# Optimization experiments

Hardware: AMD Instinct MI355X
Metric: run time of the kernel (lower is better)

The kernel has to match this reference:

```python
import jax, jax.numpy as jnp
import numpy as np

B, S, HID = 4, 1024, 1024
NH, NKV, HD = 16, 8, 64
EPS = 1e-6
ROPE_BASE = 10000.0


def setup_inputs() -> dict:
    key = jax.random.key(0)
    ks = jax.random.split(key, 6)
    hidden_states = jax.random.normal(ks[0], (B, S, HID), jnp.float32)
    # RoPE tables: cos/sin of shape [B, S, HD] (half-frequency layout, duplicated)
    inv_freq = 1.0 / (ROPE_BASE ** (jnp.arange(0, HD, 2, dtype=jnp.float32) / HD))
    pos = jnp.arange(S, dtype=jnp.float32)
    freqs = pos[:, None] * inv_freq[None, :]              # [S, HD/2]
    emb = jnp.concatenate([freqs, freqs], axis=-1)         # [S, HD]
    cos = jnp.broadcast_to(jnp.cos(emb)[None], (B, S, HD))
    sin = jnp.broadcast_to(jnp.sin(emb)[None], (B, S, HD))
    # additive causal mask [B, 1, S, S]
    causal = jnp.where(jnp.tril(jnp.ones((S, S), bool)), 0.0, -1e9).astype(jnp.float32)
    attention_mask = jnp.broadcast_to(causal[None, None], (B, 1, S, S))
    sc = 0.02
    Wq = jax.random.normal(ks[1], (NH * HD, HID), jnp.float32) * sc
    Wk = jax.random.normal(ks[2], (NKV * HD, HID), jnp.float32) * sc
    Wv = jax.random.normal(ks[3], (NKV * HD, HID), jnp.float32) * sc
    Wo = jax.random.normal(ks[4], (HID, NH * HD), jnp.float32) * sc
    q_norm_w = jnp.ones((HD,), jnp.float32)
    k_norm_w = jnp.ones((HD,), jnp.float32)
    return {"hidden_states": hidden_states, "cos": cos, "sin": sin,
            "attention_mask": attention_mask, "Wq": Wq, "Wk": Wk, "Wv": Wv,
            "Wo": Wo, "q_norm_w": q_norm_w, "k_norm_w": k_norm_w}


def _rms_norm(x, w):
    dt = x.dtype
    x32 = x.astype(jnp.float32)
    var = jnp.mean(x32 * x32, axis=-1, keepdims=True)
    x32 = x32 * jax.lax.rsqrt(var + EPS)
    return w * x32.astype(dt)


def _rotate_half(x):
    x1, x2 = jnp.split(x, 2, axis=-1)
    return jnp.concatenate([-x2, x1], axis=-1)


def reference(hidden_states, cos, sin, attention_mask, Wq, Wk, Wv, Wo, q_norm_w, k_norm_w):
    b, s, _ = hidden_states.shape
    scaling = HD ** -0.5
    # QKV projections (bias=False), reshape to heads, per-head RMSNorm on q/k
    q = (hidden_states @ Wq.T).reshape(b, s, NH, HD)
    k = (hidden_states @ Wk.T).reshape(b, s, NKV, HD)
    v = (hidden_states @ Wv.T).reshape(b, s, NKV, HD)
    q = _rms_norm(q, q_norm_w).transpose(0, 2, 1, 3)   # [B, NH, S, HD]
    k = _rms_norm(k, k_norm_w).transpose(0, 2, 1, 3)   # [B, NKV, S, HD]
    v = v.transpose(0, 2, 1, 3)                         # [B, NKV, S, HD]
    # RoPE (unsqueeze_dim=1 -> broadcast over heads)
    c = cos[:, None, :, :]
    sn = sin[:, None, :, :]
    q = q * c + _rotate_half(q) * sn
    k = k * c + _rotate_half(k) * sn
    # GQA: repeat kv heads
    groups = NH // NKV
    k = jnp.repeat(k, groups, axis=1)
    v = jnp.repeat(v, groups, axis=1)
    # eager attention
    scores = jnp.einsum('bhqd,bhkd->bhqk', q, k) * scaling + attention_mask
    attn_weights = jax.nn.softmax(scores.astype(jnp.float32), axis=-1).astype(q.dtype)
    ctx = jnp.einsum('bhqk,bhkd->bhqd', attn_weights, v)
    ctx = ctx.transpose(0, 2, 1, 3).reshape(b, s, NH * HD)
    out = ctx @ Wo.T
    return (out, attn_weights)
```

## Files before the change

kernel.cpp:

```cpp
#include <hip/hip_runtime.h>
#include <hip/hip_fp16.h>

#define Bb 4
#define Ss 1024
#define HID 1024
#define NH 16
#define NKV 8
#define HD 64

typedef _Float16 f16x8 __attribute__((ext_vector_type(8)));
typedef _Float16 f16x4 __attribute__((ext_vector_type(4)));
typedef float f32x4 __attribute__((ext_vector_type(4)));

typedef const __attribute__((address_space(1))) unsigned int gu32;
typedef __attribute__((address_space(3))) unsigned int lu32;

__device__ __forceinline__ void gl_lds16(const _Float16* g, _Float16* l) {
  __builtin_amdgcn_global_load_lds((gu32*)g, (lu32*)l, 16, 0, 0);
}

__global__ __launch_bounds__(256) void f2h_all(
    const float* __restrict__ a0, const float* __restrict__ a1,
    const float* __restrict__ a2, const float* __restrict__ a3,
    const float* __restrict__ a4, _Float16* __restrict__ o0,
    _Float16* __restrict__ o1, _Float16* __restrict__ o2,
    _Float16* __restrict__ o3, _Float16* __restrict__ o4) {
  const int bid = blockIdx.x;
  const float* src;
  _Float16* dst;
  int base;
  if (bid < 4096)      { src = a0; dst = o0; base = bid; }
  else if (bid < 5120) { src = a1; dst = o1; base = bid - 4096; }
  else if (bid < 5632) { src = a2; dst = o2; base = bid - 5120; }
  else if (bid < 6144) { src = a3; dst = o3; base = bid - 5632; }
  else                 { src = a4; dst = o4; base = bid - 6144; }
  const int i = base * 1024 + threadIdx.x * 4;
  const float4 v = *(const float4*)(src + i);
  f16x4 h;
  h[0] = (_Float16)v.x; h[1] = (_Float16)v.y;
  h[2] = (_Float16)v.z; h[3] = (_Float16)v.w;
  *(f16x4*)(dst + i) = h;
}

template <int EPI>
__global__ __launch_bounds__(256) void gemm128(
    const _Float16* __restrict__ A, const _Float16* __restrict__ Bt,
    float* __restrict__ C, _Float16* __restrict__ qh, _Float16* __restrict__ kh,
    _Float16* __restrict__ vTp, const float* __restrict__ qnw,
    const float* __restrict__ knw, const float* __restrict__ cosd,
    const float* __restrict__ sind, int N, int K) {
  __shared__ __align__(16) _Float16 As[128][64];
  __shared__ __align__(16) _Float16 Bs[128][64];
  const int tid = threadIdx.x;
  const int wave = tid >> 6, lane = tid & 63;
  const int lr = lane & 15, lk = lane >> 4;
  const int wr = wave >> 1, wc = wave & 1;
  const int bm = blockIdx.x * 128;
  const int by = blockIdx.y;
  const int bn = by * 128;

  f32x4 acc[4][4] = {};

  const _Float16* asrc[4];
  const _Float16* bsrc[4];
  _Float16 *adst[4], *bdst[4];
#pragma unroll
  for (int i = 0; i < 4; ++i) {
    const int ch = i * 256 + tid;
    const int r = ch >> 3, ccl = ch & 7;
    const int ccg = ccl ^ (r & 7);
    asrc[i] = A + (size_t)(bm + r) * K + ccg * 8;
    bsrc[i] = Bt + (size_t)(bn + r) * K + ccg * 8;
    adst[i] = &As[0][0] + ch * 8;
    bdst[i] = &Bs[0][0] + ch * 8;
  }

  for (int k0 = 0; k0 < K; k0 += 64) {
    __syncthreads();
#pragma unroll
    for (int i = 0; i < 4; ++i) {
      gl_lds16(asrc[i] + k0, adst[i]);
      gl_lds16(bsrc[i] + k0, bdst[i]);
    }
    __syncthreads();
#pragma unroll
    for (int kk = 0; kk < 2; ++kk) {
      f16x8 af[4], bf[4];
#pragma unroll
      for (int m = 0; m < 4; ++m) {
        const int r = wr * 64 + m * 16 + lr;
        const int s = (kk * 4 + lk) ^ (r & 7);
        af[m] = *(const f16x8*)(&As[r][0] + s * 8);
      }
#pragma unroll
      for (int n = 0; n < 4; ++n) {
        const int r = wc * 64 + n * 16 + lr;
        const int s = (kk * 4 + lk) ^ (r & 7);
        bf[n] = *(const f16x8*)(&Bs[r][0] + s * 8);
      }
#pragma unroll
      for (int m = 0; m < 4; ++m)
#pragma unroll
        for (int n = 0; n < 4; ++n)
          acc[m][n] =
              __builtin_amdgcn_mfma_f32_16x16x32_f16(af[m], bf[n], acc[m][n], 0, 0, 0);
    }
  }

  if (EPI == 0) {
#pragma unroll
    for (int m = 0; m < 4; ++m) {
      const int row = bm + wr * 64 + m * 16 + lk * 4;
#pragma unroll
      for (int n = 0; n < 4; ++n) {
        const int c = bn + wc * 64 + n * 16 + lr;
#pragma unroll
        for (int j = 0; j < 4; ++j)
          C[(size_t)(row + j) * N + c] = acc[m][n][j];
      }
    }
  } else {
    const int b = bm >> 10;
    const int s0 = bm & 1023;
    const int hd2 = by * 2 + wc;
    if (hd2 < 24) {
      const bool isQ = (hd2 < 16);
      const float* nw = isQ ? qnw : knw;
      _Float16* dst = isQ ? qh : kh;
      const int ncols = isQ ? (NH * HD) : (NKV * HD);
      const int hcol = (isQ ? hd2 : (hd2 - 16)) * HD;
      float nwv[4];
#pragma unroll
      for (int n = 0; n < 4; ++n) nwv[n] = nw[n * 16 + lr];
#pragma unroll
      for (int m = 0; m < 4; ++m) {
#pragma unroll
        for (int j = 0; j < 4; ++j) {
          const int row = bm + wr * 64 + m * 16 + lk * 4 + j;
          float ss = 0.f;
#pragma unroll
          for (int n = 0; n < 4; ++n) ss += acc[m][n][j] * acc[m][n][j];
#pragma unroll
          for (int o = 1; o < 16; o <<= 1) ss += __shfl_xor(ss, o);
          const float rs = rsqrtf(ss * (1.0f / 64.0f) + 1e-6f);
          float y[4];
#pragma unroll
          for (int n = 0; n < 4; ++n) y[n] = acc[m][n][j] * rs * nwv[n];
          const size_t rb = (size_t)row * HD;
#pragma unroll
          for (int n = 0; n < 4; ++n) {
            const int d = n * 16 + lr;
            const float rot = (n < 2) ? -y[n + 2] : y[n - 2];
            dst[(size_t)row * ncols + hcol + d] =
                (_Float16)(y[n] * cosd[rb + d] + rot * sind[rb + d]);
          }
        }
      }
    } else {
      const int kv = hd2 - 24;
#pragma unroll
      for (int m = 0; m < 4; ++m) {
        const int sbase = s0 + wr * 64 + m * 16 + lk * 4;
#pragma unroll
        for (int n = 0; n < 4; ++n) {
          const int d = n * 16 + lr;
          f16x4 pk;
#pragma unroll
          for (int j = 0; j < 4; ++j) pk[j] = (_Float16)acc[m][n][j];
          *(f16x4*)&vTp[((size_t)((b * NKV + kv) * HD + d)) * Ss + sbase] = pk;
        }
      }
    }
  }
}

__global__ __launch_bounds__(256) void gemm_oproj(
    const _Float16* __restrict__ A, const _Float16* __restrict__ Bt,
    float* __restrict__ C, int N, int K) {
  __shared__ __align__(16) _Float16 As[128][64];
  __shared__ __align__(16) _Float16 Bs[64][64];
  const int tid = threadIdx.x;
  const int wave = tid >> 6, lane = tid & 63;
  const int lr = lane & 15, lk = lane >> 4;
  const int bm = blockIdx.x * 128;
  const int bn = blockIdx.y * 64;

  f32x4 acc[2][4] = {};

  const _Float16* asrc[4];
  const _Float16* bsrc[2];
  _Float16 *adst[4], *bdst[2];
#pragma unroll
  for (int i = 0; i < 4; ++i) {
    const int ch = i * 256 + tid;
    const int r = ch >> 3, ccl = ch & 7;
    const int ccg = ccl ^ (r & 7);
    asrc[i] = A + (size_t)(bm + r) * K + ccg * 8;
    adst[i] = &As[0][0] + ch * 8;
  }
#pragma unroll
  for (int i = 0; i < 2; ++i) {
    const int ch = i * 256 + tid;
    const int r = ch >> 3, ccl = ch & 7;
    const int ccg = ccl ^ (r & 7);
    bsrc[i] = Bt + (size_t)(bn + r) * K + ccg * 8;
    bdst[i] = &Bs[0][0] + ch * 8;
  }

  for (int k0 = 0; k0 < K; k0 += 64) {
    __syncthreads();
#pragma unroll
    for (int i = 0; i < 4; ++i) gl_lds16(asrc[i] + k0, adst[i]);
#pragma unroll
    for (int i = 0; i < 2; ++i) gl_lds16(bsrc[i] + k0, bdst[i]);
    __syncthreads();
#pragma unroll
    for (int kk = 0; kk < 2; ++kk) {
      f16x8 af[2], bf[4];
#pragma unroll
      for (int m = 0; m < 2; ++m) {
        const int r = wave * 32 + m * 16 + lr;
        const int s = (kk * 4 + lk) ^ (r & 7);
        af[m] = *(const f16x8*)(&As[r][0] + s * 8);
      }
#pragma unroll
      for (int n = 0; n < 4; ++n) {
        const int r = n * 16 + lr;
        const int s = (kk * 4 + lk) ^ (r & 7);
        bf[n] = *(const f16x8*)(&Bs[r][0] + s * 8);
      }
#pragma unroll
      for (int m = 0; m < 2; ++m)
#pragma unroll
        for (int n = 0; n < 4; ++n)
          acc[m][n] =
              __builtin_amdgcn_mfma_f32_16x16x32_f16(af[m], bf[n], acc[m][n], 0, 0, 0);
    }
  }
#pragma unroll
  for (int m = 0; m < 2; ++m) {
    const int row = bm + wave * 32 + m * 16 + lk * 4;
#pragma unroll
    for (int n = 0; n < 4; ++n) {
      const int c = bn + n * 16 + lr;
#pragma unroll
      for (int j = 0; j < 4; ++j)
        C[(size_t)(row + j) * N + c] = acc[m][n][j];
    }
  }
}

__global__ __launch_bounds__(256) void attn_kernel(
    const _Float16* __restrict__ qh, const _Float16* __restrict__ kh,
    const _Float16* __restrict__ vT, float* __restrict__ attn,
    _Float16* __restrict__ ctxh) {
  __shared__ __align__(16) _Float16 Ks[64][72];
  __shared__ __align__(16) _Float16 Vs[64][72];
  __shared__ __align__(16) _Float16 Wh[4][16][72];
  const int x = blockIdx.x, h = blockIdx.y, b = blockIdx.z;
  int qt;
  switch (b) {
    case 0:  qt = x; break;
    case 1:  qt = 15 - x; break;
    case 2:  qt = (x + 8) & 15; break;
    default: qt = (7 - x) & 15; break;
  }
  const int kvh = h >> 1;
  const int tid = threadIdx.x, wave = tid >> 6, lane = tid & 63;
  const int lr = lane & 15, lk = lane >> 4;
  const int q0 = qt * 64, qrow0 = q0 + wave * 16;
  float* attn_bh = attn + (size_t)(b * NH + h) * Ss * Ss;

  const int sr = tid >> 3, sc = tid & 7;
  const _Float16* kb0 = kh + (size_t)(b * Ss) * (NKV * HD) + kvh * HD + sc * 8;
  const _Float16* vb0 = vT + (size_t)((b * NKV + kvh) * HD) * Ss + sc * 8;

  const _Float16* qp = qh + (size_t)(b * Ss + qrow0 + lr) * (NH * HD) + h * HD + lk * 8;
  const f16x8 aq0 = *(const f16x8*)qp;
  const f16x8 aq1 = *(const f16x8*)(qp + 32);

  const float C1 = 0.18033688011112042f;
  const float C2 = -11.541560327111707f;

  f16x8 pk0 = *(const f16x8*)(kb0 + (size_t)sr * (NKV * HD));
  f16x8 pk1 = *(const f16x8*)(kb0 + (size_t)(sr + 32) * (NKV * HD));
  float lsum[4] = {0.f, 0.f, 0.f, 0.f};
  for (int t = 0; t <= qt; ++t) {
    __syncthreads();
    *(f16x8*)&Ks[sr][sc * 8] = pk0;
    *(f16x8*)&Ks[sr + 32][sc * 8] = pk1;
    if (t < qt) {
      pk0 = *(const f16x8*)(kb0 + (size_t)((t + 1) * 64 + sr) * (NKV * HD));
      pk1 = *(const f16x8*)(kb0 + (size_t)((t + 1) * 64 + sr + 32) * (NKV * HD));
    }
    __syncthreads();
    f32x4 acc[4] = {};
#pragma unroll
    for (int n = 0; n < 4; ++n) {
      f16x8 b0 = *(const f16x8*)&Ks[n * 16 + lr][lk * 8];
      acc[n] = __builtin_amdgcn_mfma_f32_16x16x32_f16(aq0, b0, acc[n], 0, 0, 0);
    }
#pragma unroll
    for (int n = 0; n < 4; ++n) {
      f16x8 b1 = *(const f16x8*)&Ks[n * 16 + lr][32 + lk * 8];
      acc[n] = __builtin_amdgcn_mfma_f32_16x16x32_f16(aq1, b1, acc[n], 0, 0, 0);
    }
    if (t < qt) {
#pragma unroll
      for (int j = 0; j < 4; ++j)
#pragma unroll
        for (int n = 0; n < 4; ++n) lsum[j] += exp2f(fmaf(acc[n][j], C1, C2));
    } else {
#pragma unroll
      for (int j = 0; j < 4; ++j) {
        const int gr = qrow0 + lk * 4 + j;
#pragma unroll
        for (int n = 0; n < 4; ++n) {
          float p = exp2f(fmaf(acc[n][j], C1, C2));
          if (q0 + n * 16 + lr > gr) p = 0.f;
          lsum[j] += p;
        }
      }
    }
  }
  float linv[4];
#pragma unroll
  for (int j = 0; j < 4; ++j) {
#pragma unroll
    for (int o = 1; o < 16; o <<= 1) lsum[j] += __shfl_xor(lsum[j], o);
    linv[j] = 1.0f / lsum[j];
  }

  pk0 = *(const f16x8*)(kb0 + (size_t)sr * (NKV * HD));
  pk1 = *(const f16x8*)(kb0 + (size_t)(sr + 32) * (NKV * HD));
  f16x8 pv0 = *(const f16x8*)(vb0 + (size_t)sr * Ss);
  f16x8 pv1 = *(const f16x8*)(vb0 + (size_t)(sr + 32) * Ss);
  f32x4 acc2[4] = {};
  const int wr2 = lane >> 4;
  const int wc2 = (lane & 15) * 4;
  for (int t = 0; t <= qt; ++t) {
    __syncthreads();
    *(f16x8*)&Ks[sr][sc * 8] = pk0;
    *(f16x8*)&Ks[sr + 32][sc * 8] = pk1;
    *(f16x8*)&Vs[sr][sc * 8] = pv0;
    *(f16x8*)&Vs[sr + 32][sc * 8] = pv1;
    if (t < qt) {
      pk0 = *(const f16x8*)(kb0 + (size_t)((t + 1) * 64 + sr) * (NKV * HD));
      pk1 = *(const f16x8*)(kb0 + (size_t)((t + 1) * 64 + sr + 32) * (NKV * HD));
      pv0 = *(const f16x8*)(vb0 + (size_t)sr * Ss + (t + 1) * 64);
      pv1 = *(const f16x8*)(vb0 + (size_t)(sr + 32) * Ss + (t + 1) * 64);
    }
    __syncthreads();
    f32x4 acc[4] = {};
#pragma unroll
    for (int n = 0; n < 4; ++n) {
      f16x8 b0 = *(const f16x8*)&Ks[n * 16 + lr][lk * 8];
      acc[n] = __builtin_amdgcn_mfma_f32_16x16x32_f16(aq0, b0, acc[n], 0, 0, 0);
    }
#pragma unroll
    for (int n = 0; n < 4; ++n) {
      f16x8 b1 = *(const f16x8*)&Ks[n * 16 + lr][32 + lk * 8];
      acc[n] = __builtin_amdgcn_mfma_f32_16x16x32_f16(aq1, b1, acc[n], 0, 0, 0);
    }
    if (t < qt) {
#pragma unroll
      for (int j = 0; j < 4; ++j)
#pragma unroll
        for (int n = 0; n < 4; ++n) {
          const float w = exp2f(fmaf(acc[n][j], C1, C2)) * linv[j];
          Wh[wave][lk * 4 + j][n * 16 + lr] = (_Float16)w;
        }
    } else {
#pragma unroll
      for (int j = 0; j < 4; ++j) {
        const int gr = qrow0 + lk * 4 + j;
#pragma unroll
        for (int n = 0; n < 4; ++n) {
          float w = exp2f(fmaf(acc[n][j], C1, C2)) * linv[j];
          if (q0 + n * 16 + lr > gr) w = 0.f;
          Wh[wave][lk * 4 + j][n * 16 + lr] = (_Float16)w;
        }
      }
    }
#pragma unroll
    for (int kc = 0; kc < 2; ++kc) {
      f16x8 aw = *(const f16x8*)&Wh[wave][lr][kc * 32 + lk * 8];
#pragma unroll
      for (int n = 0; n < 4; ++n) {
        f16x8 bv = *(const f16x8*)&Vs[n * 16 + lr][kc * 32 + lk * 8];
        acc2[n] = __builtin_amdgcn_mfma_f32_16x16x32_f16(aw, bv, acc2[n], 0, 0, 0);
      }
    }
#pragma unroll
    for (int i2 = 0; i2 < 4; ++i2) {
      f16x4 hv = *(const f16x4*)&Wh[wave][wr2 + i2 * 4][wc2];
      *(float4*)&attn_bh[(size_t)(qrow0 + wr2 + i2 * 4) * Ss + t * 64 + wc2] =
          make_float4((float)hv[0], (float)hv[1], (float)hv[2], (float)hv[3]);
    }
  }

  for (int t = qt + 1; t < 16; ++t)
    for (int idx = tid; idx < 1024; idx += 256) {
      int r = idx >> 4, c4 = (idx & 15) * 4;
      *(float4*)&attn_bh[(size_t)(q0 + r) * Ss + t * 64 + c4] =
          make_float4(0.f, 0.f, 0.f, 0.f);
    }

#pragma unroll
  for (int n = 0; n < 4; ++n)
#pragma unroll
    for (int j = 0; j < 4; ++j)
      ctxh[(size_t)(b * Ss + qrow0 + lk * 4 + j) * (NH * HD) + h * HD + n * 16 + lr] =
          (_Float16)acc2[n][j];
}

extern "C" void kernel_launch(void* const* d_in, const int* in_sizes, int n_in,
                              void* d_out, int out_size, void* d_ws, size_t ws_size,
                              hipStream_t stream) {
  const float* hs   = (const float*)d_in[0];
  const float* cosb = (const float*)d_in[1];
  const float* sinb = (const float*)d_in[2];
  const float* Wq = (const float*)d_in[4];
  const float* Wk = (const float*)d_in[5];
  const float* Wv = (const float*)d_in[6];
  const float* Wo = (const float*)d_in[7];
  const float* qw = (const float*)d_in[8];
  const float* kw = (const float*)d_in[9];

  char* ws = (char*)d_ws;
  _Float16* Xh    = (_Float16*)(ws);
  _Float16* Wqkvh = (_Float16*)(ws + 8388608);
  _Float16* Woh   = (_Float16*)(ws + 12582912);
  _Float16* qh    = (_Float16*)(ws + 14680064);
  _Float16* kh    = (_Float16*)(ws + 23068672);
  _Float16* vT    = (_Float16*)(ws + 27262976);
  _Float16* ctxh  = (_Float16*)(ws + 31457280);

  float* out  = (float*)d_out;
  float* attn = out + (size_t)Bb * Ss * HID;

  f2h_all<<<7168, 256, 0, stream>>>(hs, Wq, Wk, Wv, Wo, Xh, Wqkvh,
                                    Wqkvh + 1048576, Wqkvh + 1572864, Woh);

  gemm128<1><<<dim3(32, 16), 256, 0, stream>>>(
      Xh, Wqkvh, nullptr, qh, kh, vT, qw, kw, cosb, sinb, 2048, 1024);

  attn_kernel<<<dim3(16, 16, 4), 256, 0, stream>>>(qh, kh, vT, attn, ctxh);

  gemm_oproj<<<dim3(32, 16), 256, 0, stream>>>(ctxh, Woh, out, 1024, 1024);
}
```

Before: 132.4 us.

## Share K/V tiles across GQA head pair in one 512-thread attention block

```diff
diff --git a/kernel.cpp b/kernel.cpp
--- a/kernel.cpp
+++ b/kernel.cpp
@@ -250,30 +250,30 @@
   }
 }
 
-__global__ __launch_bounds__(256) void attn_kernel(
+__global__ __launch_bounds__(512) void attn_kernel(
     const _Float16* __restrict__ qh, const _Float16* __restrict__ kh,
     const _Float16* __restrict__ vT, float* __restrict__ attn,
     _Float16* __restrict__ ctxh) {
   __shared__ __align__(16) _Float16 Ks[64][72];
   __shared__ __align__(16) _Float16 Vs[64][72];
-  __shared__ __align__(16) _Float16 Wh[4][16][72];
-  const int x = blockIdx.x, h = blockIdx.y, b = blockIdx.z;
+  __shared__ __align__(16) _Float16 Wh[8][16][72];
+  const int x = blockIdx.x, g = blockIdx.y, b = blockIdx.z;
   int qt;
   switch (b) {
     case 0:  qt = x; break;
-    case 1:  qt = 15 - x; break;
-    case 2:  qt = (x + 8) & 15; break;
+    case 1:  qt = (x + 8) & 15; break;
+    case 2:  qt = 15 - x; break;
     default: qt = (7 - x) & 15; break;
   }
-  const int kvh = h >> 1;
   const int tid = threadIdx.x, wave = tid >> 6, lane = tid & 63;
   const int lr = lane & 15, lk = lane >> 4;
-  const int q0 = qt * 64, qrow0 = q0 + wave * 16;
+  const int h = 2 * g + (wave >> 2);
+  const int q0 = qt * 64, qrow0 = q0 + (wave & 3) * 16;
   float* attn_bh = attn + (size_t)(b * NH + h) * Ss * Ss;
 
   const int sr = tid >> 3, sc = tid & 7;
-  const _Float16* kb0 = kh + (size_t)(b * Ss) * (NKV * HD) + kvh * HD + sc * 8;
-  const _Float16* vb0 = vT + (size_t)((b * NKV + kvh) * HD) * Ss + sc * 8;
+  const _Float16* kb0 = kh + (size_t)(b * Ss) * (NKV * HD) + g * HD + sc * 8;
+  const _Float16* vb0 = vT + (size_t)((b * NKV + g) * HD) * Ss + sc * 8;
 
   const _Float16* qp = qh + (size_t)(b * Ss + qrow0 + lr) * (NH * HD) + h * HD + lk * 8;
   const f16x8 aq0 = *(const f16x8*)qp;
@@ -282,17 +282,13 @@
   const float C1 = 0.18033688011112042f;
   const float C2 = -11.541560327111707f;
 
-  f16x8 pk0 = *(const f16x8*)(kb0 + (size_t)sr * (NKV * HD));
-  f16x8 pk1 = *(const f16x8*)(kb0 + (size_t)(sr + 32) * (NKV * HD));
+  f16x8 pk = *(const f16x8*)(kb0 + (size_t)sr * (NKV * HD));
   float lsum[4] = {0.f, 0.f, 0.f, 0.f};
   for (int t = 0; t <= qt; ++t) {
     __syncthreads();
-    *(f16x8*)&Ks[sr][sc * 8] = pk0;
-    *(f16x8*)&Ks[sr + 32][sc * 8] = pk1;
-    if (t < qt) {
-      pk0 = *(const f16x8*)(kb0 + (size_t)((t + 1) * 64 + sr) * (NKV * HD));
-      pk1 = *(const f16x8*)(kb0 + (size_t)((t + 1) * 64 + sr + 32) * (NKV * HD));
-    }
+    *(f16x8*)&Ks[sr][sc * 8] = pk;
+    if (t < qt)
+      pk = *(const f16x8*)(kb0 + (size_t)((t + 1) * 64 + sr) * (NKV * HD));
     __syncthreads();
     f32x4 acc[4] = {};
 #pragma unroll
@@ -331,24 +327,18 @@
     linv[j] = 1.0f / lsum[j];
   }
 
-  pk0 = *(const f16x8*)(kb0 + (size_t)sr * (NKV * HD));
-  pk1 = *(const f16x8*)(kb0 + (size_t)(sr + 32) * (NKV * HD));
-  f16x8 pv0 = *(const f16x8*)(vb0 + (size_t)sr * Ss);
-  f16x8 pv1 = *(const f16x8*)(vb0 + (size_t)(sr + 32) * Ss);
+  pk = *(const f16x8*)(kb0 + (size_t)sr * (NKV * HD));
+  f16x8 pv = *(const f16x8*)(vb0 + (size_t)sr * Ss);
   f32x4 acc2[4] = {};
   const int wr2 = lane >> 4;
   const int wc2 = (lane & 15) * 4;
   for (int t = 0; t <= qt; ++t) {
     __syncthreads();
-    *(f16x8*)&Ks[sr][sc * 8] = pk0;
-    *(f16x8*)&Ks[sr + 32][sc * 8] = pk1;
-    *(f16x8*)&Vs[sr][sc * 8] = pv0;
-    *(f16x8*)&Vs[sr + 32][sc * 8] = pv1;
+    *(f16x8*)&Ks[sr][sc * 8] = pk;
+    *(f16x8*)&Vs[sr][sc * 8] = pv;
     if (t < qt) {
-      pk0 = *(const f16x8*)(kb0 + (size_t)((t + 1) * 64 + sr) * (NKV * HD));
-      pk1 = *(const f16x8*)(kb0 + (size_t)((t + 1) * 64 + sr + 32) * (NKV * HD));
-      pv0 = *(const f16x8*)(vb0 + (size_t)sr * Ss + (t + 1) * 64);
-      pv1 = *(const f16x8*)(vb0 + (size_t)(sr + 32) * Ss + (t + 1) * 64);
+      pk = *(const f16x8*)(kb0 + (size_t)((t + 1) * 64 + sr) * (NKV * HD));
+      pv = *(const f16x8*)(vb0 + (size_t)sr * Ss + (t + 1) * 64);
     }
     __syncthreads();
     f32x4 acc[4] = {};
@@ -399,12 +389,16 @@
     }
   }
 
-  for (int t = qt + 1; t < 16; ++t)
-    for (int idx = tid; idx < 1024; idx += 256) {
-      int r = idx >> 4, c4 = (idx & 15) * 4;
-      *(float4*)&attn_bh[(size_t)(q0 + r) * Ss + t * 64 + c4] =
-          make_float4(0.f, 0.f, 0.f, 0.f);
-    }
+  {
+    float* attn_z = attn + (size_t)(b * NH + 2 * g + (tid >> 8)) * Ss * Ss;
+    const int tz = tid & 255;
+    for (int t = qt + 1; t < 16; ++t)
+      for (int idx = tz; idx < 1024; idx += 256) {
+        int r = idx >> 4, c4 = (idx & 15) * 4;
+        *(float4*)&attn_z[(size_t)(q0 + r) * Ss + t * 64 + c4] =
+            make_float4(0.f, 0.f, 0.f, 0.f);
+      }
+  }
 
 #pragma unroll
   for (int n = 0; n < 4; ++n)
@@ -445,7 +439,7 @@
   gemm128<1><<<dim3(32, 16), 256, 0, stream>>>(
       Xh, Wqkvh, nullptr, qh, kh, vT, qw, kw, cosb, sinb, 2048, 1024);
 
-  attn_kernel<<<dim3(16, 16, 4), 256, 0, stream>>>(qh, kh, vT, attn, ctxh);
+  attn_kernel<<<dim3(16, 8, 4), 512, 0, stream>>>(qh, kh, vT, attn, ctxh);
 
   gemm_oproj<<<dim3(32, 16), 256, 0, stream>>>(ctxh, Woh, out, 1024, 1024);
 }
```

After: 128.5 us. -3.0%, faster.
